# Kernel optimization log

Hardware: AMD Instinct MI355X
Metric: run time of the kernel (lower is better)

The kernel has to match this reference:

```python
import jax, jax.numpy as jnp
import numpy as np

NUM_BINS = 256
SMOOTH = 1e-06
EPS = 1e-06

_LAPLACIAN = jnp.array([[0., 1., 0.], [1., -4., 1.], [0., 1., 0.]], dtype=jnp.float32).reshape(1, 1, 3, 3)


def _histogram(x, bins):
    # torch.bucketize(x, bins) (right=False) == searchsorted side='left'; then -1.
    B = x.shape[0]
    flat = x.reshape(B, -1)
    idx = jnp.searchsorted(bins, flat, side='left') - 1  # [B, N], -1 possible for x==0
    hist = jnp.zeros((B, NUM_BINS), dtype=jnp.float32)
    # single-pass scatter-add; out-of-range (-1) indices dropped, matching the torch
    # loop which only counts bins 0..255
    hist = hist.at[jnp.arange(B)[:, None], idx].add(1.0, mode='drop')
    return (hist + SMOOTH) / (hist.sum(axis=1, keepdims=True) + SMOOTH)


def _histogram_loss(enhanced_y, original_y):
    bins = jnp.linspace(0.0, 1.0, NUM_BINS + 1)
    h_e = _histogram(enhanced_y, bins)
    h_o = _histogram(original_y, bins)
    return jnp.mean((h_e - h_o) ** 2) / NUM_BINS


def _mean_contrast(img):
    c = jax.lax.conv_general_dilated(img, _LAPLACIAN, window_strides=(1, 1), padding=((1, 1), (1, 1)))
    return jnp.mean(jnp.abs(c))


def _contrast_loss(enhanced_y, original_y):
    c_e = _mean_contrast(enhanced_y)
    c_o = _mean_contrast(original_y)
    return jnp.abs(c_e - c_o) / (c_o + EPS)


def _smoothness_loss(image):
    dx = image[:, :, 1:, :] - image[:, :, :-1, :]
    dy = image[:, :, :, 1:] - image[:, :, :, :-1]
    return jnp.mean(jnp.abs(dx)) + jnp.mean(jnp.abs(dy))


def setup_inputs() -> dict:
    key = jax.random.key(0)
    k1, k2 = jax.random.split(key)
    B, C, H, W = 32, 1, 1024, 1024
    enhanced_y = jax.random.uniform(k1, (B, C, H, W), dtype=jnp.float32)
    original_y = jax.random.uniform(k2, (B, C, H, W), dtype=jnp.float32)
    return {"enhanced_y": enhanced_y, "original_y": original_y}


def reference(enhanced_y, original_y):
    l1 = jnp.mean(jnp.abs(enhanced_y - original_y))
    hist = _histogram_loss(enhanced_y, original_y)
    cont = _contrast_loss(enhanced_y, original_y)
    smooth = _smoothness_loss(enhanced_y)
    return l1 + 0.1 * hist + 0.1 * cont + 0.01 * smooth
```

## Files before the change

kernel.cpp:

```cpp
#include <hip/hip_runtime.h>

#define HH 1024
#define WW 1024
#define NBATCH 32
#define ROWS 32
#define NBINS 256

__device__ inline int bin_of(float x) {
    float t = x * 256.0f;
    int it = (int)t;
    if ((float)it == t) it -= 1;
    return it;
}

__device__ inline float wave_red(float v) {
    #pragma unroll
    for (int off = 32; off > 0; off >>= 1) v += __shfl_down(v, off);
    return v;
}

__global__ __launch_bounds__(256, 4) void fused_main(
    const float* __restrict__ E, const float* __restrict__ O,
    unsigned int* __restrict__ gHistE, unsigned int* __restrict__ gHistO,
    double* __restrict__ sums)
{
    const int bt = blockIdx.y;
    const int r0 = blockIdx.x * ROWS;
    const float* __restrict__ e = E + (size_t)bt * HH * WW;
    const float* __restrict__ o = O + (size_t)bt * HH * WW;

    __shared__ unsigned int hE[NBINS];
    __shared__ unsigned int hO[NBINS];
    __shared__ float rbuf[4][5];

    const int tid  = threadIdx.x;
    hE[tid] = 0u;
    hO[tid] = 0u;
    __syncthreads();

    const int lane = tid & 63;
    const int wv   = tid >> 6;
    const int c    = tid * 4;
    const bool edgeL    = (lane == 0);
    const bool edgeR    = (lane == 63);
    const bool hasRight = (c + 4 < WW);

    float prvE[4], prvO[4], curE[4], curO[4];
    {
        const float4 a = *reinterpret_cast<const float4*>(e + (size_t)r0 * WW + c);
        curE[0]=a.x; curE[1]=a.y; curE[2]=a.z; curE[3]=a.w;
        const float4 b = *reinterpret_cast<const float4*>(o + (size_t)r0 * WW + c);
        curO[0]=b.x; curO[1]=b.y; curO[2]=b.z; curO[3]=b.w;
        if (r0 > 0) {
            const float4 p = *reinterpret_cast<const float4*>(e + (size_t)(r0-1) * WW + c);
            prvE[0]=p.x; prvE[1]=p.y; prvE[2]=p.z; prvE[3]=p.w;
            const float4 q = *reinterpret_cast<const float4*>(o + (size_t)(r0-1) * WW + c);
            prvO[0]=q.x; prvO[1]=q.y; prvO[2]=q.z; prvO[3]=q.w;
        } else {
            #pragma unroll
            for (int j = 0; j < 4; ++j) { prvE[j] = 0.f; prvO[j] = 0.f; }
        }
    }

    float accL1 = 0.f, accLapE = 0.f, accLapO = 0.f, accDx = 0.f, accDy = 0.f;

    for (int r = r0; r < r0 + ROWS; ++r) {
        const int rn = r + 1;
        float nxtE[4], nxtO[4];
        if (rn < HH) {
            const float4 a = *reinterpret_cast<const float4*>(e + (size_t)rn * WW + c);
            nxtE[0]=a.x; nxtE[1]=a.y; nxtE[2]=a.z; nxtE[3]=a.w;
            const float4 b = *reinterpret_cast<const float4*>(o + (size_t)rn * WW + c);
            nxtO[0]=b.x; nxtO[1]=b.y; nxtO[2]=b.z; nxtO[3]=b.w;
        } else {
            #pragma unroll
            for (int j = 0; j < 4; ++j) { nxtE[j] = 0.f; nxtO[j] = 0.f; }
        }

        float lE = __shfl_up(curE[3], 1);
        float rE = __shfl_down(curE[0], 1);
        float lO = __shfl_up(curO[3], 1);
        float rO = __shfl_down(curO[0], 1);
        if (edgeL) {
            lE = (c > 0) ? e[(size_t)r * WW + c - 1] : 0.f;
            lO = (c > 0) ? o[(size_t)r * WW + c - 1] : 0.f;
        }
        if (edgeR) {
            rE = hasRight ? e[(size_t)r * WW + c + 4] : 0.f;
            rO = hasRight ? o[(size_t)r * WW + c + 4] : 0.f;
        }

        #pragma unroll
        for (int j = 0; j < 4; ++j) {
            const float le = (j == 0) ? lE : curE[j-1];
            const float re = (j == 3) ? rE : curE[j+1];
            accLapE += fabsf(prvE[j] + nxtE[j] + le + re - 4.f * curE[j]);
            const float lo = (j == 0) ? lO : curO[j-1];
            const float ro = (j == 3) ? rO : curO[j+1];
            accLapO += fabsf(prvO[j] + nxtO[j] + lo + ro - 4.f * curO[j]);
            accL1 += fabsf(curE[j] - curO[j]);
            const int be = bin_of(curE[j]);
            if (be >= 0 && be < NBINS) atomicAdd(&hE[be], 1u);
            const int bo = bin_of(curO[j]);
            if (bo >= 0 && bo < NBINS) atomicAdd(&hO[bo], 1u);
        }

        if (rn < HH) {
            #pragma unroll
            for (int j = 0; j < 4; ++j) accDx += fabsf(nxtE[j] - curE[j]);
        }
        accDy += fabsf(curE[1]-curE[0]) + fabsf(curE[2]-curE[1]) + fabsf(curE[3]-curE[2]);
        if (hasRight) accDy += fabsf(rE - curE[3]);

        #pragma unroll
        for (int j = 0; j < 4; ++j) {
            prvE[j] = curE[j]; curE[j] = nxtE[j];
            prvO[j] = curO[j]; curO[j] = nxtO[j];
        }
    }

    float acc[5] = {accL1, accLapE, accLapO, accDx, accDy};
    #pragma unroll
    for (int k = 0; k < 5; ++k) {
        const float w = wave_red(acc[k]);
        if (lane == 0) rbuf[wv][k] = w;
    }
    __syncthreads();
    if (tid == 0) {
        #pragma unroll
        for (int k = 0; k < 5; ++k) {
            const double tot = (double)rbuf[0][k] + rbuf[1][k] + rbuf[2][k] + rbuf[3][k];
            atomicAdd(&sums[k], tot);
        }
    }

    atomicAdd(&gHistE[bt * NBINS + tid], hE[tid]);
    atomicAdd(&gHistO[bt * NBINS + tid], hO[tid]);
}

__global__ __launch_bounds__(256) void finalize(
    const unsigned int* __restrict__ gHistE, const unsigned int* __restrict__ gHistO,
    const double* __restrict__ sums, float* __restrict__ out)
{
    __shared__ double sred[8];
    const int tid  = threadIdx.x;
    const int lane = tid & 63;
    const int wv   = tid >> 6;

    double hacc = 0.0;
    for (int bt = 0; bt < NBATCH; ++bt) {
        const double ce = (double)gHistE[bt * NBINS + tid];
        const double co = (double)gHistO[bt * NBINS + tid];
        double te = ce, to = co;
        #pragma unroll
        for (int off = 32; off > 0; off >>= 1) {
            te += __shfl_down(te, off);
            to += __shfl_down(to, off);
        }
        if (lane == 0) { sred[wv] = te; sred[4 + wv] = to; }
        __syncthreads();
        te = sred[0] + sred[1] + sred[2] + sred[3];
        to = sred[4] + sred[5] + sred[6] + sred[7];
        __syncthreads();
        const double he = (ce + 1e-6) / (te + 1e-6);
        const double ho = (co + 1e-6) / (to + 1e-6);
        const double d  = he - ho;
        hacc += d * d;
    }
    #pragma unroll
    for (int off = 32; off > 0; off >>= 1) hacc += __shfl_down(hacc, off);
    if (lane == 0) sred[wv] = hacc;
    __syncthreads();

    if (tid == 0) {
        const double hsum  = sred[0] + sred[1] + sred[2] + sred[3];
        const double hist  = hsum / ((double)NBATCH * NBINS) / (double)NBINS;
        const double N     = (double)NBATCH * HH * WW;
        const double l1    = sums[0] / N;
        const double cE    = sums[1] / N;
        const double cO    = sums[2] / N;
        const double cont  = fabs(cE - cO) / (cO + 1e-6);
        const double dxm   = sums[3] / ((double)NBATCH * (HH - 1) * WW);
        const double dym   = sums[4] / ((double)NBATCH * HH * (WW - 1));
        out[0] = (float)(l1 + 0.1 * hist + 0.1 * cont + 0.01 * (dxm + dym));
    }
}

extern "C" void kernel_launch(void* const* d_in, const int* in_sizes, int n_in,
                              void* d_out, int out_size, void* d_ws, size_t ws_size,
                              hipStream_t stream)
{
    const float* E = (const float*)d_in[0];
    const float* O = (const float*)d_in[1];
    float* out = (float*)d_out;

    unsigned int* gHistE = (unsigned int*)d_ws;
    unsigned int* gHistO = gHistE + NBATCH * NBINS;
    double* sums = (double*)((char*)d_ws + (size_t)2 * NBATCH * NBINS * sizeof(unsigned int));

    hipMemsetAsync(d_ws, 0,
                   (size_t)2 * NBATCH * NBINS * sizeof(unsigned int) + 8 * sizeof(double),
                   stream);

    dim3 grid(HH / ROWS, NBATCH);
    fused_main<<<grid, 256, 0, stream>>>(E, O, gHistE, gHistO, sums);
    finalize<<<1, 256, 0, stream>>>(gHistE, gHistO, sums, out);
}
```

Measured before the change: 352.9 us.

## Prefetch rows two ahead, privatize LDS histograms, and spread global atomics

The row loop now keeps two extra rows in flight as a software prefetch, and loads each row's edge halo values one iteration early. The shared histograms are replicated into 8 slots per bin to cut LDS atomic contention, and the slots are summed before the global add. Per-batch global sum slots reduce contention on the five double atomics. The finalize kernel computes per-batch totals once instead of resynchronising in every loop iteration. The cost is more registers and 16KB of LDS per block, which may lower occupancy.

```diff
diff --git a/kernel.cpp b/kernel.cpp
--- a/kernel.cpp
+++ b/kernel.cpp
@@ -5,6 +5,7 @@
 #define NBATCH 32
 #define ROWS 32
 #define NBINS 256
+#define NSLOT 8
 
 __device__ inline int bin_of(float x) {
     float t = x * 256.0f;
@@ -13,7 +14,7 @@
     return it;
 }
 
-__device__ inline float wave_red(float v) {
+__device__ inline float wave_red_f(float v) {
     #pragma unroll
     for (int off = 32; off > 0; off >>= 1) v += __shfl_down(v, off);
     return v;
@@ -29,66 +30,68 @@
     const float* __restrict__ e = E + (size_t)bt * HH * WW;
     const float* __restrict__ o = O + (size_t)bt * HH * WW;
 
-    __shared__ unsigned int hE[NBINS];
-    __shared__ unsigned int hO[NBINS];
+    __shared__ unsigned int hE[NBINS * NSLOT];
+    __shared__ unsigned int hO[NBINS * NSLOT];
     __shared__ float rbuf[4][5];
 
-    const int tid  = threadIdx.x;
-    hE[tid] = 0u;
-    hO[tid] = 0u;
+    const int tid = threadIdx.x;
+    #pragma unroll
+    for (int i = 0; i < (NBINS * NSLOT) / 256; ++i) {
+        hE[tid + i * 256] = 0u;
+        hO[tid + i * 256] = 0u;
+    }
     __syncthreads();
 
     const int lane = tid & 63;
     const int wv   = tid >> 6;
+    const int slot = tid & (NSLOT - 1);
     const int c    = tid * 4;
     const bool edgeL    = (lane == 0);
     const bool edgeR    = (lane == 63);
     const bool hasRight = (c + 4 < WW);
 
-    float prvE[4], prvO[4], curE[4], curO[4];
-    {
-        const float4 a = *reinterpret_cast<const float4*>(e + (size_t)r0 * WW + c);
-        curE[0]=a.x; curE[1]=a.y; curE[2]=a.z; curE[3]=a.w;
-        const float4 b = *reinterpret_cast<const float4*>(o + (size_t)r0 * WW + c);
-        curO[0]=b.x; curO[1]=b.y; curO[2]=b.z; curO[3]=b.w;
-        if (r0 > 0) {
-            const float4 p = *reinterpret_cast<const float4*>(e + (size_t)(r0-1) * WW + c);
-            prvE[0]=p.x; prvE[1]=p.y; prvE[2]=p.z; prvE[3]=p.w;
-            const float4 q = *reinterpret_cast<const float4*>(o + (size_t)(r0-1) * WW + c);
-            prvO[0]=q.x; prvO[1]=q.y; prvO[2]=q.z; prvO[3]=q.w;
+    auto loadrow = [&](const float* __restrict__ p, int r, float v[4]) {
+        const float4 a = *reinterpret_cast<const float4*>(p + (size_t)r * WW + c);
+        v[0] = a.x; v[1] = a.y; v[2] = a.z; v[3] = a.w;
+    };
+
+    float prvE[4] = {0,0,0,0}, prvO[4] = {0,0,0,0};
+    float curE[4], curO[4], nxtE[4], nxtO[4], p1E[4], p1O[4];
+    if (r0 > 0) { loadrow(e, r0 - 1, prvE); loadrow(o, r0 - 1, prvO); }
+    loadrow(e, r0,     curE); loadrow(o, r0,     curO);
+    loadrow(e, r0 + 1, nxtE); loadrow(o, r0 + 1, nxtO);
+    loadrow(e, r0 + 2, p1E);  loadrow(o, r0 + 2, p1O);
+
+    float lEc = 0.f, rEc = 0.f, lOc = 0.f, rOc = 0.f;
+    if (edgeL && c > 0)    { lEc = e[(size_t)r0 * WW + c - 1]; lOc = o[(size_t)r0 * WW + c - 1]; }
+    if (edgeR && hasRight) { rEc = e[(size_t)r0 * WW + c + 4]; rOc = o[(size_t)r0 * WW + c + 4]; }
+
+    float accL1 = 0.f, accLapE = 0.f, accLapO = 0.f, accDx = 0.f, accDy = 0.f;
+
+    for (int k = 0; k < ROWS; ++k) {
+        const int r = r0 + k;
+
+        float p2E[4], p2O[4];
+        if (k + 3 <= ROWS && r + 3 < HH) {
+            loadrow(e, r + 3, p2E); loadrow(o, r + 3, p2O);
         } else {
             #pragma unroll
-            for (int j = 0; j < 4; ++j) { prvE[j] = 0.f; prvO[j] = 0.f; }
-        }
-    }
-
-    float accL1 = 0.f, accLapE = 0.f, accLapO = 0.f, accDx = 0.f, accDy = 0.f;
-
-    for (int r = r0; r < r0 + ROWS; ++r) {
-        const int rn = r + 1;
-        float nxtE[4], nxtO[4];
-        if (rn < HH) {
-            const float4 a = *reinterpret_cast<const float4*>(e + (size_t)rn * WW + c);
-            nxtE[0]=a.x; nxtE[1]=a.y; nxtE[2]=a.z; nxtE[3]=a.w;
-            const float4 b = *reinterpret_cast<const float4*>(o + (size_t)rn * WW + c);
-            nxtO[0]=b.x; nxtO[1]=b.y; nxtO[2]=b.z; nxtO[3]=b.w;
-        } else {
-            #pragma unroll
-            for (int j = 0; j < 4; ++j) { nxtE[j] = 0.f; nxtO[j] = 0.f; }
+            for (int j = 0; j < 4; ++j) { p2E[j] = 0.f; p2O[j] = 0.f; }
+        }
+
+        float lEn = 0.f, rEn = 0.f, lOn = 0.f, rOn = 0.f;
+        if (k + 1 < ROWS) {
+            const int rn = r + 1;
+            if (edgeL && c > 0)    { lEn = e[(size_t)rn * WW + c - 1]; lOn = o[(size_t)rn * WW + c - 1]; }
+            if (edgeR && hasRight) { rEn = e[(size_t)rn * WW + c + 4]; rOn = o[(size_t)rn * WW + c + 4]; }
         }
 
         float lE = __shfl_up(curE[3], 1);
         float rE = __shfl_down(curE[0], 1);
         float lO = __shfl_up(curO[3], 1);
         float rO = __shfl_down(curO[0], 1);
-        if (edgeL) {
-            lE = (c > 0) ? e[(size_t)r * WW + c - 1] : 0.f;
-            lO = (c > 0) ? o[(size_t)r * WW + c - 1] : 0.f;
-        }
-        if (edgeR) {
-            rE = hasRight ? e[(size_t)r * WW + c + 4] : 0.f;
-            rO = hasRight ? o[(size_t)r * WW + c + 4] : 0.f;
-        }
+        if (edgeL) { lE = lEc; lO = lOc; }
+        if (edgeR) { rE = rEc; rO = rOc; }
 
         #pragma unroll
         for (int j = 0; j < 4; ++j) {
@@ -100,12 +103,12 @@
             accLapO += fabsf(prvO[j] + nxtO[j] + lo + ro - 4.f * curO[j]);
             accL1 += fabsf(curE[j] - curO[j]);
             const int be = bin_of(curE[j]);
-            if (be >= 0 && be < NBINS) atomicAdd(&hE[be], 1u);
+            if (be >= 0 && be < NBINS) atomicAdd(&hE[be * NSLOT + slot], 1u);
             const int bo = bin_of(curO[j]);
-            if (bo >= 0 && bo < NBINS) atomicAdd(&hO[bo], 1u);
-        }
-
-        if (rn < HH) {
+            if (bo >= 0 && bo < NBINS) atomicAdd(&hO[bo * NSLOT + slot], 1u);
+        }
+
+        if (r + 1 < HH) {
             #pragma unroll
             for (int j = 0; j < 4; ++j) accDx += fabsf(nxtE[j] - curE[j]);
         }
@@ -114,74 +117,101 @@
 
         #pragma unroll
         for (int j = 0; j < 4; ++j) {
-            prvE[j] = curE[j]; curE[j] = nxtE[j];
-            prvO[j] = curO[j]; curO[j] = nxtO[j];
-        }
+            prvE[j] = curE[j]; curE[j] = nxtE[j]; nxtE[j] = p1E[j]; p1E[j] = p2E[j];
+            prvO[j] = curO[j]; curO[j] = nxtO[j]; nxtO[j] = p1O[j]; p1O[j] = p2O[j];
+        }
+        lEc = lEn; rEc = rEn; lOc = lOn; rOc = rOn;
     }
 
     float acc[5] = {accL1, accLapE, accLapO, accDx, accDy};
     #pragma unroll
-    for (int k = 0; k < 5; ++k) {
-        const float w = wave_red(acc[k]);
-        if (lane == 0) rbuf[wv][k] = w;
+    for (int kk = 0; kk < 5; ++kk) {
+        const float w = wave_red_f(acc[kk]);
+        if (lane == 0) rbuf[wv][kk] = w;
     }
     __syncthreads();
     if (tid == 0) {
         #pragma unroll
-        for (int k = 0; k < 5; ++k) {
-            const double tot = (double)rbuf[0][k] + rbuf[1][k] + rbuf[2][k] + rbuf[3][k];
-            atomicAdd(&sums[k], tot);
-        }
-    }
-
-    atomicAdd(&gHistE[bt * NBINS + tid], hE[tid]);
-    atomicAdd(&gHistO[bt * NBINS + tid], hO[tid]);
+        for (int kk = 0; kk < 5; ++kk) {
+            const double tot = (double)rbuf[0][kk] + rbuf[1][kk] + rbuf[2][kk] + rbuf[3][kk];
+            atomicAdd(&sums[bt * 5 + kk], tot);
+        }
+    }
+
+    unsigned int se = 0u, so = 0u;
+    #pragma unroll
+    for (int s = 0; s < NSLOT; ++s) {
+        se += hE[tid * NSLOT + s];
+        so += hO[tid * NSLOT + s];
+    }
+    atomicAdd(&gHistE[bt * NBINS + tid], se);
+    atomicAdd(&gHistO[bt * NBINS + tid], so);
 }
 
 __global__ __launch_bounds__(256) void finalize(
     const unsigned int* __restrict__ gHistE, const unsigned int* __restrict__ gHistO,
     const double* __restrict__ sums, float* __restrict__ out)
 {
-    __shared__ double sred[8];
+    __shared__ double teL[NBATCH], toL[NBATCH];
+    __shared__ double red[4];
     const int tid  = threadIdx.x;
     const int lane = tid & 63;
     const int wv   = tid >> 6;
+
+    #pragma unroll
+    for (int i = 0; i < NBATCH / 4; ++i) {
+        const int bt = wv * (NBATCH / 4) + i;
+        const uint4 a = *reinterpret_cast<const uint4*>(&gHistE[bt * NBINS + lane * 4]);
+        const uint4 b = *reinterpret_cast<const uint4*>(&gHistO[bt * NBINS + lane * 4]);
+        unsigned int te = a.x + a.y + a.z + a.w;
+        unsigned int to = b.x + b.y + b.z + b.w;
+        #pragma unroll
+        for (int off = 32; off > 0; off >>= 1) {
+            te += __shfl_down(te, off);
+            to += __shfl_down(to, off);
+        }
+        if (lane == 0) { teL[bt] = (double)te; toL[bt] = (double)to; }
+    }
+    __syncthreads();
 
     double hacc = 0.0;
     for (int bt = 0; bt < NBATCH; ++bt) {
         const double ce = (double)gHistE[bt * NBINS + tid];
         const double co = (double)gHistO[bt * NBINS + tid];
-        double te = ce, to = co;
-        #pragma unroll
-        for (int off = 32; off > 0; off >>= 1) {
-            te += __shfl_down(te, off);
-            to += __shfl_down(to, off);
-        }
-        if (lane == 0) { sred[wv] = te; sred[4 + wv] = to; }
-        __syncthreads();
-        te = sred[0] + sred[1] + sred[2] + sred[3];
-        to = sred[4] + sred[5] + sred[6] + sred[7];
-        __syncthreads();
-        const double he = (ce + 1e-6) / (te + 1e-6);
-        const double ho = (co + 1e-6) / (to + 1e-6);
+        const double he = (ce + 1e-6) / (teL[bt] + 1e-6);
+        const double ho = (co + 1e-6) / (toL[bt] + 1e-6);
         const double d  = he - ho;
         hacc += d * d;
     }
     #pragma unroll
     for (int off = 32; off > 0; off >>= 1) hacc += __shfl_down(hacc, off);
-    if (lane == 0) sred[wv] = hacc;
+    if (lane == 0) red[wv] = hacc;
+
+    double s0 = 0, s1 = 0, s2 = 0, s3 = 0, s4 = 0;
+    if (wv == 0) {
+        if (lane < NBATCH) {
+            s0 = sums[lane * 5 + 0]; s1 = sums[lane * 5 + 1]; s2 = sums[lane * 5 + 2];
+            s3 = sums[lane * 5 + 3]; s4 = sums[lane * 5 + 4];
+        }
+        #pragma unroll
+        for (int off = 32; off > 0; off >>= 1) {
+            s0 += __shfl_down(s0, off); s1 += __shfl_down(s1, off);
+            s2 += __shfl_down(s2, off); s3 += __shfl_down(s3, off);
+            s4 += __shfl_down(s4, off);
+        }
+    }
     __syncthreads();
 
     if (tid == 0) {
-        const double hsum  = sred[0] + sred[1] + sred[2] + sred[3];
-        const double hist  = hsum / ((double)NBATCH * NBINS) / (double)NBINS;
-        const double N     = (double)NBATCH * HH * WW;
-        const double l1    = sums[0] / N;
-        const double cE    = sums[1] / N;
-        const double cO    = sums[2] / N;
-        const double cont  = fabs(cE - cO) / (cO + 1e-6);
-        const double dxm   = sums[3] / ((double)NBATCH * (HH - 1) * WW);
-        const double dym   = sums[4] / ((double)NBATCH * HH * (WW - 1));
+        const double hsum = red[0] + red[1] + red[2] + red[3];
+        const double hist = hsum / ((double)NBATCH * NBINS) / (double)NBINS;
+        const double N    = (double)NBATCH * HH * WW;
+        const double l1   = s0 / N;
+        const double cE   = s1 / N;
+        const double cO   = s2 / N;
+        const double cont = fabs(cE - cO) / (cO + 1e-6);
+        const double dxm  = s3 / ((double)NBATCH * (HH - 1) * WW);
+        const double dym  = s4 / ((double)NBATCH * HH * (WW - 1));
         out[0] = (float)(l1 + 0.1 * hist + 0.1 * cont + 0.01 * (dxm + dym));
     }
 }
@@ -199,7 +229,8 @@
     double* sums = (double*)((char*)d_ws + (size_t)2 * NBATCH * NBINS * sizeof(unsigned int));
 
     hipMemsetAsync(d_ws, 0,
-                   (size_t)2 * NBATCH * NBINS * sizeof(unsigned int) + 8 * sizeof(double),
+                   (size_t)2 * NBATCH * NBINS * sizeof(unsigned int)
+                   + (size_t)NBATCH * 5 * sizeof(double),
                    stream);
 
     dim3 grid(HH / ROWS, NBATCH);
```

Result: faster. 297.4 us (-15.7%).
